# Optimization experiments

Measured on AMD Instinct MI355X. Metric: run time of the kernel, lower is better.

## Reference

```python
import jax, jax.numpy as jnp
import numpy as np

B, H, W, C = 16, 64, 64, 128
P0, P1 = 2, 2  # pool_size


def setup_inputs() -> dict:
    key = jax.random.key(0)
    k_val, k_dh, k_dw = jax.random.split(key, 3)
    val = jax.random.normal(k_val, (B, H, W, C), dtype=jnp.float32)
    # Emulate tf.nn.max_pool_with_argmax indices (flat index into the unpooled
    # tensor, batch offset included): unique, in-range, one per pooled element.
    dh = jax.random.randint(k_dh, (B, H, W, C), 0, P0)
    dw = jax.random.randint(k_dw, (B, H, W, C), 0, P1)
    bb = jnp.arange(B)[:, None, None, None]
    hh = jnp.arange(H)[None, :, None, None]
    ww = jnp.arange(W)[None, None, :, None]
    cc = jnp.arange(C)[None, None, None, :]
    H2, W2 = H * P0, W * P1
    mask = (bb * (H2 * W2 * C)
            + (P0 * hh + dh) * (W2 * C)
            + (P1 * ww + dw) * C
            + cc).astype(jnp.int64)
    return {"val": val, "mask": mask}


def reference(val, mask):
    b, h, w, c = val.shape
    per_batch = h * w * c * P0 * P1  # = (h*P0)*(w*P1)*c
    val_flat = val.reshape(-1)
    # batch id per flat element (matches the broadcast batch_range in the original)
    b_flat = jnp.repeat(jnp.arange(b), h * w * c)
    local = mask.reshape(-1) - b_flat.astype(mask.dtype) * per_batch
    # tf.scatter_nd sums duplicates; argmax indices are unique so .add is faithful
    ans = jnp.zeros((b, per_batch), dtype=val.dtype).at[b_flat, local].add(val_flat)
    return ans.reshape(b, h * P0, w * P1, c)
```

## Files before the change

### kernel.cpp

```cpp
#include <hip/hip_runtime.h>


constexpr int B  = 16;
constexpr int H  = 64;
constexpr int W  = 64;
constexpr int C  = 128;
constexpr int H2 = 128;
constexpr int W2 = 128;
constexpr int NOUT = B * H2 * W2 * C;

__global__ __launch_bounds__(256)
void unpool_gather_kernel(const float* __restrict__ val,
                          const int*   __restrict__ mask,
                          float*       __restrict__ out)
{
    int t   = blockIdx.x * blockDim.x + threadIdx.x;
    int idx = t << 2;
    if (idx >= NOUT) return;

    int c    = idx & (C - 1);
    int rest = idx >> 7;
    int x    = rest & (W2 - 1);
    rest   >>= 7;
    int y    = rest & (H2 - 1);
    int b    = rest >> 7;

    int h = y >> 1;
    int w = x >> 1;
    int moff = ((b * H + h) * W + w) * C + c;

    const int4   m = *reinterpret_cast<const int4*>(mask + moff);
    const float4 v = *reinterpret_cast<const float4*>(val  + moff);

    float4 o;
    o.x = (m.x == idx + 0) ? v.x : 0.0f;
    o.y = (m.y == idx + 1) ? v.y : 0.0f;
    o.z = (m.z == idx + 2) ? v.z : 0.0f;
    o.w = (m.w == idx + 3) ? v.w : 0.0f;

    *reinterpret_cast<float4*>(out + idx) = o;
}

extern "C" void kernel_launch(void* const* d_in, const int* in_sizes, int n_in,
                              void* d_out, int out_size, void* d_ws, size_t ws_size,
                              hipStream_t stream)
{
    const float* val  = (const float*)d_in[0];
    const int*   mask = (const int*)d_in[1];
    float*       out  = (float*)d_out;

    const int n_threads = NOUT / 4;
    const int block = 256;
    const int grid  = n_threads / block;
    unpool_gather_kernel<<<grid, block, 0, stream>>>(val, mask, out);
}
```

Before: 36.34 us.

## Switch unpool from per-output gather to per-window scatter with nontemporal stores

Each thread now reads one vector of 4 pooled values and their mask entries, then writes all four positions of the 2x2 output window. It no longer reads each input four times as the output-indexed gather did. The window position is decoded straight from the mask's bits (dh from bit 14, dw from bit 7), which assumes every index lies inside its own pooling window, as argmax indices do. Output stores are marked nontemporal so the large write stream does not pollute the caches.

```diff
diff --git a/kernel.cpp b/kernel.cpp
--- a/kernel.cpp
+++ b/kernel.cpp
@@ -1,5 +1,8 @@
 #include <hip/hip_runtime.h>
 
+
+typedef float f32x4 __attribute__((ext_vector_type(4)));
+typedef int   i32x4 __attribute__((ext_vector_type(4)));
 
 constexpr int B  = 16;
 constexpr int H  = 64;
@@ -7,38 +10,47 @@
 constexpr int C  = 128;
 constexpr int H2 = 128;
 constexpr int W2 = 128;
-constexpr int NOUT = B * H2 * W2 * C;
+constexpr int NPOOL = B * H * W * C;
 
 __global__ __launch_bounds__(256)
-void unpool_gather_kernel(const float* __restrict__ val,
+void unpool_window_kernel(const float* __restrict__ val,
                           const int*   __restrict__ mask,
                           float*       __restrict__ out)
 {
-    int t   = blockIdx.x * blockDim.x + threadIdx.x;
-    int idx = t << 2;
-    if (idx >= NOUT) return;
+    int t    = blockIdx.x * blockDim.x + threadIdx.x;
+    int moff = t << 2;
 
-    int c    = idx & (C - 1);
-    int rest = idx >> 7;
-    int x    = rest & (W2 - 1);
-    rest   >>= 7;
-    int y    = rest & (H2 - 1);
-    int b    = rest >> 7;
+    int w = (moff >> 7)  & (W - 1);
+    int h = (moff >> 13) & (H - 1);
+    int b =  moff >> 19;
+    int c =  moff & (C - 1);
 
-    int h = y >> 1;
-    int w = x >> 1;
-    int moff = ((b * H + h) * W + w) * C + c;
+    const i32x4 m = *reinterpret_cast<const i32x4*>(mask + moff);
+    const f32x4 v = *reinterpret_cast<const f32x4*>(val  + moff);
 
-    const int4   m = *reinterpret_cast<const int4*>(mask + moff);
-    const float4 v = *reinterpret_cast<const float4*>(val  + moff);
+    int s0 = ((m.x >> 13) & 2) | ((m.x >> 7) & 1);
+    int s1 = ((m.y >> 13) & 2) | ((m.y >> 7) & 1);
+    int s2 = ((m.z >> 13) & 2) | ((m.z >> 7) & 1);
+    int s3 = ((m.w >> 13) & 2) | ((m.w >> 7) & 1);
 
-    float4 o;
-    o.x = (m.x == idx + 0) ? v.x : 0.0f;
-    o.y = (m.y == idx + 1) ? v.y : 0.0f;
-    o.z = (m.z == idx + 2) ? v.z : 0.0f;
-    o.w = (m.w == idx + 3) ? v.w : 0.0f;
+    f32x4 q00, q01, q10, q11;
+    q00.x = (s0 == 0) ? v.x : 0.0f;  q01.x = (s0 == 1) ? v.x : 0.0f;
+    q10.x = (s0 == 2) ? v.x : 0.0f;  q11.x = (s0 == 3) ? v.x : 0.0f;
+    q00.y = (s1 == 0) ? v.y : 0.0f;  q01.y = (s1 == 1) ? v.y : 0.0f;
+    q10.y = (s1 == 2) ? v.y : 0.0f;  q11.y = (s1 == 3) ? v.y : 0.0f;
+    q00.z = (s2 == 0) ? v.z : 0.0f;  q01.z = (s2 == 1) ? v.z : 0.0f;
+    q10.z = (s2 == 2) ? v.z : 0.0f;  q11.z = (s2 == 3) ? v.z : 0.0f;
+    q00.w = (s3 == 0) ? v.w : 0.0f;  q01.w = (s3 == 1) ? v.w : 0.0f;
+    q10.w = (s3 == 2) ? v.w : 0.0f;  q11.w = (s3 == 3) ? v.w : 0.0f;
 
-    *reinterpret_cast<float4*>(out + idx) = o;
+    int base = (((b * H2 + 2 * h) * W2) + 2 * w) * C + c;
+    float* p00 = out + base;
+    float* p10 = p00 + W2 * C;
+
+    __builtin_nontemporal_store(q00, reinterpret_cast<f32x4*>(p00));
+    __builtin_nontemporal_store(q01, reinterpret_cast<f32x4*>(p00 + C));
+    __builtin_nontemporal_store(q10, reinterpret_cast<f32x4*>(p10));
+    __builtin_nontemporal_store(q11, reinterpret_cast<f32x4*>(p10 + C));
 }
 
 extern "C" void kernel_launch(void* const* d_in, const int* in_sizes, int n_in,
@@ -49,8 +61,8 @@
     const int*   mask = (const int*)d_in[1];
     float*       out  = (float*)d_out;
 
-    const int n_threads = NOUT / 4;
+    const int n_threads = NPOOL / 4;
     const int block = 256;
     const int grid  = n_threads / block;
-    unpool_gather_kernel<<<grid, block, 0, stream>>>(val, mask, out);
+    unpool_window_kernel<<<grid, block, 0, stream>>>(val, mask, out);
 }
```

After: 33.62 us. -7.5%, faster.
